# Performance work log

Measured on AMD Instinct MI355X. Metric: run time of the kernel, lower is better.

The kernel has to match this reference:

```python
import jax, jax.numpy as jnp
import numpy as np

K = 10      # neighbors; conv width math 10 -> 3 -> 1
EPS = 1e-5  # InstanceNorm2d default eps (affine=False)
NEG = 0.2   # leaky relu slope


def _instnorm(x):
    m = x.mean(axis=(2, 3), keepdims=True)
    v = x.var(axis=(2, 3), keepdims=True)  # biased var, as in torch instance_norm
    return (x - m) * jax.lax.rsqrt(v + EPS)


def _conv13(x, w, b, s):
    y = jax.lax.conv_general_dilated(x, w, (1, s), 'VALID',
                                     dimension_numbers=('NCHW', 'OIHW', 'NCHW'))
    return y + b[None, :, None, None]


def _block(x, wA, bA, wB, bB):
    # Sequential(conv(1,3,stride(1,3)), IN, ReLU, conv(1,3), IN, ReLU)
    y = jax.nn.relu(_instnorm(_conv13(x, wA, bA, 3)))
    return jax.nn.relu(_instnorm(_conv13(y, wB, bB, 1)))


def _knn_idx(coords, k):
    # coords [B,2,N] -> k nearest neighbor indices [B,N,k] (self excluded)
    pts = coords.transpose(0, 2, 1)
    sq = (pts ** 2).sum(-1)
    dist = sq[:, :, None] + sq[:, None, :] - 2.0 * jnp.einsum('bnc,bmc->bnm', pts, pts)
    dist = jnp.clip(dist, 1e-12)
    _, idx = jax.lax.top_k(-dist, k + 1)  # smallest distances, sorted
    return idx[:, :, 1:]


def _gather_nb(x, idx):
    # x [B,C,N], idx [B,N,k] -> [B,C,N,k]
    return jax.vmap(lambda f, i: f[:, i])(x, idx)


def _graph_feat(feats, idx):
    nb = _gather_nb(feats, idx)
    ctr = jnp.broadcast_to(feats[..., None], nb.shape)
    return jnp.concatenate([ctr, nb - ctr], axis=1)  # [B,2C,N,k]


def _cos_angle(coords, idx):
    nei = _gather_nb(coords, idx)          # [B,2,N,k]
    ctr = coords[..., None]                # [B,2,N,1]
    dot = (ctr * nei).sum(axis=1, keepdims=True)
    na = jnp.sqrt((ctr ** 2).sum(axis=1, keepdims=True))
    nb = jnp.sqrt((nei ** 2).sum(axis=1, keepdims=True))
    return dot / (na * nb)                 # [B,1,N,k]


def _c1(w, x):
    # 1x1 conv, no bias
    return jnp.einsum('oi,bihw->bohw', w, x)


def _forward(coords, features, W1, W2, W3, W3o, a1wA, a1bA, a1wB, a1bB,
             a2wA, a2bA, a2wB, a2bB, angwA, angbA, angwB, angbB):
    B, C, N = features.shape
    lrelu = lambda x: jax.nn.leaky_relu(x, NEG)
    x0 = features[..., None]
    # KNN depends only on coords: all three torch graph builds give identical indices
    idx = _knn_idx(coords, K)
    x1_old = _graph_feat(features, idx)                         # [B,2C,N,K]
    x1 = _block(x1_old, a1wA, a1bA, a1wB, a1bB)                 # [B,C,N,1]
    # angle_enc1 is shared and idx identical -> f_ang1 == f_ang2
    f_ang = _block(_cos_angle(coords, idx), angwA, angbA, angwB, angbB)
    x2 = _block(_graph_feat(x1[..., 0], idx), a2wA, a2bA, a2wB, a2bB)
    x3 = jnp.concatenate([x0, x1 + f_ang, x2 + f_ang], axis=1)  # [B,3C,N,1]
    x3 = lrelu(_instnorm(_c1(W3, x3))).reshape(B, -1, N)
    x1o = lrelu(_instnorm(_c1(W1, x1_old))).max(axis=-1, keepdims=True)   # [B,C,N,1]
    x2o = lrelu(_instnorm(_c1(W2, _graph_feat(x1o[..., 0], idx)))).max(axis=-1, keepdims=True)
    x3o = jnp.concatenate([x0, x1o, x2o], axis=1)               # [B,4C,N,1]
    x3o = lrelu(_instnorm(_c1(W3o, x3o))).reshape(B, -1, N)
    return x3 + x3o


def setup_inputs():
    key = jax.random.key(0)
    ks = jax.random.split(key, 20)
    B, C, N = 4, 128, 4096
    r = lambda i, shp, sc=1.0: jax.random.normal(ks[i], shp, jnp.float32) * sc
    s = 0.05
    return {
        'coords': r(0, (B, 2, N)),
        'features': r(1, (B, C, N)),
        'W1': r(2, (C, 2 * C), s),
        'W2': r(3, (2 * C, 2 * C), s),
        'W3': r(4, (C, 3 * C), s),
        'W3o': r(5, (C, 4 * C), s),
        'a1wA': r(6, (C, 2 * C, 1, 3), s), 'a1bA': r(7, (C,), s),
        'a1wB': r(8, (C, C, 1, 3), s), 'a1bB': r(9, (C,), s),
        'a2wA': r(10, (C, 2 * C, 1, 3), s), 'a2bA': r(11, (C,), s),
        'a2wB': r(12, (C, C, 1, 3), s), 'a2bB': r(13, (C,), s),
        'angwA': r(14, (C, 1, 1, 3), s), 'angbA': r(15, (C,), s),
        'angwB': r(16, (C, C, 1, 3), s), 'angbB': r(17, (C,), s),
    }


def reference(coords, features, W1, W2, W3, W3o, a1wA, a1bA, a1wB, a1bB,
              a2wA, a2bA, a2wB, a2bB, angwA, angbA, angwB, angbB):
    return _forward(coords, features, W1, W2, W3, W3o, a1wA, a1bA, a1wB, a1bB,
                    a2wA, a2bA, a2wB, a2bB, angwA, angbA, angwB, angbB)
```

## Files before the change

kernel.cpp:

```cpp
#include <hip/hip_runtime.h>
#include <hip/hip_bf16.h>

typedef unsigned long long ull;

#define BN 4
#define CH 128
#define NP 4096
#define KNB 10
#define EPSI 1e-5f
#define GM_PTS 16
#define CA_PTS 8

#define FMA4(A, W, F) do { (A).x += (W).x*(F); (A).y += (W).y*(F); \
                           (A).z += (W).z*(F); (A).w += (W).w*(F); } while(0)

__device__ __forceinline__ ull shfl_xor_u64(ull v, int mask) {
    unsigned lo = (unsigned)(v & 0xFFFFFFFFu);
    unsigned hi = (unsigned)(v >> 32);
    lo = __shfl_xor(lo, mask);
    hi = __shfl_xor(hi, mask);
    return ((ull)hi << 32) | lo;
}

__device__ __forceinline__ int clampj(int j) { return ((unsigned)j < (unsigned)NP) ? j : 0; }

__device__ __forceinline__ void d_packA(const float* w, float* WT, int i) {
    int co = i % CH, ci = (i / CH) % CH, s = i / (CH * CH);
    float val;
    if (s == 0) {
        val = 0.f;
        for (int dk = 0; dk < 3; dk++)
            val += w[(co * 256 + ci) * 3 + dk] - w[(co * 256 + 128 + ci) * 3 + dk];
    } else {
        val = w[(co * 256 + 128 + ci) * 3 + (s - 1)];
    }
    WT[i] = val;
}
__device__ __forceinline__ void d_packB(const float* w, float* WT, int i) {
    int co = i % CH, ci = (i / CH) % CH, dk = i / (CH * CH);
    WT[i] = w[(co * CH + ci) * 3 + dk];
}
__device__ __forceinline__ void d_packUV(const float* w, float* Wu, float* Wn, int Cout, int i) {
    int co = i % Cout, ci = i / Cout;
    float a = w[co * 256 + ci], bb = w[co * 256 + 128 + ci];
    Wu[i] = a - bb; Wn[i] = bb;
}
__device__ __forceinline__ void d_packP(const float* w, float* WT, int Cin, int Cout, int i) {
    int co = i % Cout, ci = i / Cout;
    WT[i] = w[co * Cin + ci];
}

__global__ void pack_all(const float* __restrict__ a1wA, const float* __restrict__ a2wA,
                         const float* __restrict__ a1wB, const float* __restrict__ a2wB,
                         const float* __restrict__ angwB, const float* __restrict__ W1,
                         const float* __restrict__ W2, const float* __restrict__ W3,
                         const float* __restrict__ W3o, const float* __restrict__ angwA,
                         float* __restrict__ WA1T, float* __restrict__ WA2T,
                         float* __restrict__ WB1T, float* __restrict__ WB2T,
                         float* __restrict__ WBAT,
                         float* __restrict__ W1U, float* __restrict__ W1N,
                         float* __restrict__ W2U, float* __restrict__ W2N,
                         float* __restrict__ W3T, float* __restrict__ W3OT,
                         float* __restrict__ WANGA) {
    int i = blockIdx.x * 256 + threadIdx.x;
    const int sA = 4 * CH * CH;
    const int sB = 3 * CH * CH;
    if (i < sA) { d_packA(a1wA, WA1T, i); return; } i -= sA;
    if (i < sA) { d_packA(a2wA, WA2T, i); return; } i -= sA;
    if (i < sB) { d_packB(a1wB, WB1T, i); return; } i -= sB;
    if (i < sB) { d_packB(a2wB, WB2T, i); return; } i -= sB;
    if (i < sB) { d_packB(angwB, WBAT, i); return; } i -= sB;
    if (i < CH * CH) { d_packUV(W1, W1U, W1N, CH, i); return; } i -= CH * CH;
    if (i < CH * 256) { d_packUV(W2, W2U, W2N, 256, i); return; } i -= CH * 256;
    if (i < 384 * CH) { d_packP(W3, W3T, 384, CH, i); return; } i -= 384 * CH;
    if (i < 512 * CH) { d_packP(W3o, W3OT, 512, CH, i); return; } i -= 512 * CH;
    if (i < 3 * CH) { d_packP(angwA, WANGA, 3, CH, i); return; }
}

__global__ void ftrans_kernel(const float* __restrict__ feats, float* __restrict__ F) {
    int i = blockIdx.x * 256 + threadIdx.x;
    if (i >= BN * CH * NP) return;
    int n = i % NP, c = (i / NP) % CH, b = i / (NP * CH);
    F[(b * NP + n) * CH + c] = feats[i];
}

__global__ void knn_kernel(const float* __restrict__ coords, int* __restrict__ IDX) {
    int gw = blockIdx.x * 4 + (threadIdx.x >> 6);
    int b = gw / NP;
    int n = gw % NP;
    int lane = threadIdx.x & 63;
    float xn = coords[(b * 2 + 0) * NP + n];
    float yn = coords[(b * 2 + 1) * NP + n];
    float sn = __fadd_rn(__fmul_rn(xn, xn), __fmul_rn(yn, yn));
    ull a[11];
    #pragma unroll
    for (int q = 0; q < 11; q++) a[q] = 0xFFFFFFFFFFFFFFFFULL;
    for (int m = lane; m < NP; m += 64) {
        float xm = coords[(b * 2 + 0) * NP + m];
        float ym = coords[(b * 2 + 1) * NP + m];
        float sm = __fadd_rn(__fmul_rn(xm, xm), __fmul_rn(ym, ym));
        float dot = __fmaf_rn(yn, ym, __fmul_rn(xn, xm));
        float d = __fsub_rn(__fadd_rn(sn, sm), __fmul_rn(2.0f, dot));
        d = fmaxf(d, 1e-12f);
        ull key = ((ull)__float_as_uint(d) << 32) | (unsigned)m;
        if (key < a[10]) {
            a[10] = key;
            #pragma unroll
            for (int q = 10; q > 0; --q)
                if (a[q] < a[q - 1]) { ull t = a[q]; a[q] = a[q - 1]; a[q - 1] = t; }
        }
    }
    for (int r = 0; r < 11; ++r) {
        ull k = a[0];
        ull mk = k;
        #pragma unroll
        for (int off = 1; off < 64; off <<= 1) {
            ull o = shfl_xor_u64(mk, off);
            mk = (o < mk) ? o : mk;
        }
        if (k == mk) {
            #pragma unroll
            for (int q = 0; q < 10; ++q) a[q] = a[q + 1];
            a[10] = 0xFFFFFFFFFFFFFFFFULL;
        }
        if (lane == 0 && r > 0) IDX[(b * NP + n) * KNB + (r - 1)] = (int)(mk & 0xFFFFFFFFu);
    }
}

__global__ void cosangle_kernel(const float* __restrict__ coords, const int* __restrict__ IDX,
                                float* __restrict__ COSA) {
    int i = blockIdx.x * 256 + threadIdx.x;
    if (i >= BN * NP * KNB) return;
    int n = (i / KNB) % NP, b = i / (KNB * NP);
    int j = clampj(IDX[i]);
    float xc = coords[(b * 2 + 0) * NP + n], yc = coords[(b * 2 + 1) * NP + n];
    float xm = coords[(b * 2 + 0) * NP + j], ym = coords[(b * 2 + 1) * NP + j];
    float dot = xc * xm + yc * ym;
    float na = sqrtf(xc * xc + yc * yc);
    float nb2 = sqrtf(xm * xm + ym * ym);
    COSA[i] = dot / fmaxf(na * nb2, 1e-30f);
}

__global__ __launch_bounds__(256) void convA_kernel(const float* __restrict__ Fin,
                             const int* __restrict__ IDX,
                             const float* __restrict__ WT, float* __restrict__ YA,
                             float* __restrict__ PART,
                             const float* __restrict__ STATS, int slot) {
    __shared__ __align__(16) float ctr[CA_PTS][CH];
    __shared__ __align__(16) float nb[CA_PTS][9][CH];
    __shared__ int jidx[CA_PTS * 9];
    int b = blockIdx.x / (NP / CA_PTS);
    int chunk = blockIdx.x % (NP / CA_PTS);
    int n0 = chunk * CA_PTS;
    int cog = threadIdx.x & 31;
    int pg  = threadIdx.x >> 5;
    const float* SB = (slot >= 0) ? &STATS[((size_t)(slot * BN + b) * 256) * 2] : nullptr;
    if (threadIdx.x < CA_PTS * 9) {
        int n = threadIdx.x / 9, kk = threadIdx.x % 9;
        jidx[threadIdx.x] = clampj(IDX[(b * NP + n0 + n) * KNB + kk]);
    }
    __syncthreads();
    {
        int v4 = threadIdx.x;
        int n = v4 >> 5, c4 = v4 & 31;
        float4 x = *(const float4*)&Fin[(size_t)(b * NP + n0 + n) * CH + c4 * 4];
        if (SB) {
            float4 s0 = *(const float4*)&SB[c4 * 8];
            float4 s1 = *(const float4*)&SB[c4 * 8 + 4];
            x.x = fmaxf((x.x - s0.x) * s0.y, 0.f);
            x.y = fmaxf((x.y - s0.z) * s0.w, 0.f);
            x.z = fmaxf((x.z - s1.x) * s1.y, 0.f);
            x.w = fmaxf((x.w - s1.z) * s1.w, 0.f);
        }
        *(float4*)&ctr[n][c4 * 4] = x;
    }
    for (int v4 = threadIdx.x; v4 < CA_PTS * 9 * 32; v4 += 256) {
        int n = v4 / 288, rem = v4 % 288, kk = rem >> 5, c4 = rem & 31;
        float4 x = *(const float4*)&Fin[(size_t)(b * NP + jidx[n * 9 + kk]) * CH + c4 * 4];
        if (SB) {
            float4 s0 = *(const float4*)&SB[c4 * 8];
            float4 s1 = *(const float4*)&SB[c4 * 8 + 4];
            x.x = fmaxf((x.x - s0.x) * s0.y, 0.f);
            x.y = fmaxf((x.y - s0.z) * s0.w, 0.f);
            x.z = fmaxf((x.z - s1.x) * s1.y, 0.f);
            x.w = fmaxf((x.w - s1.z) * s1.w, 0.f);
        }
        *(float4*)&nb[n][kk][c4 * 4] = x;
    }
    __syncthreads();
    const float4* W4 = (const float4*)WT;
    float4 cacc; cacc.x = cacc.y = cacc.z = cacc.w = 0.f;
    {
        const float* xb = &ctr[pg][0];
        for (int ci = 0; ci < CH; ci += 4) {
            float4 x = *(const float4*)&xb[ci];
            #pragma unroll
            for (int u = 0; u < 4; ++u) {
                float4 w = W4[(ci + u) * 32 + cog];
                float f = ((const float*)&x)[u];
                FMA4(cacc, w, f);
            }
        }
    }
    float4 t0 = cacc, t1 = cacc, t2 = cacc;
    for (int dk = 0; dk < 3; ++dk) {
        const float4* Wd = W4 + (size_t)(1 + dk) * (CH * 32);
        const float* b0 = &nb[pg][0 * 3 + dk][0];
        const float* b1 = &nb[pg][1 * 3 + dk][0];
        const float* b2 = &nb[pg][2 * 3 + dk][0];
        for (int ci = 0; ci < CH; ci += 4) {
            float4 x0 = *(const float4*)&b0[ci];
            float4 x1 = *(const float4*)&b1[ci];
            float4 x2 = *(const float4*)&b2[ci];
            #pragma unroll
            for (int u = 0; u < 4; ++u) {
                float4 w = Wd[(ci + u) * 32 + cog];
                float f0 = ((const float*)&x0)[u];
                float f1 = ((const float*)&x1)[u];
                float f2 = ((const float*)&x2)[u];
                FMA4(t0, w, f0); FMA4(t1, w, f1); FMA4(t2, w, f2);
            }
        }
    }
    {
        size_t base = ((size_t)(b * NP + n0 + pg) * 3) * CH + cog * 4;
        *(float4*)&YA[base + 0 * CH] = t0;
        *(float4*)&YA[base + 1 * CH] = t1;
        *(float4*)&YA[base + 2 * CH] = t2;
    }
    float s4[4], q4[4];
    s4[0] = t0.x + t1.x + t2.x; q4[0] = t0.x*t0.x + t1.x*t1.x + t2.x*t2.x;
    s4[1] = t0.y + t1.y + t2.y; q4[1] = t0.y*t0.y + t1.y*t1.y + t2.y*t2.y;
    s4[2] = t0.z + t1.z + t2.z; q4[2] = t0.z*t0.z + t1.z*t1.z + t2.z*t2.z;
    s4[3] = t0.w + t1.w + t2.w; q4[3] = t0.w*t0.w + t1.w*t1.w + t2.w*t2.w;
    __syncthreads();
    float* red = &nb[0][0][0];
    #pragma unroll
    for (int j = 0; j < 4; ++j) {
        red[((pg * 32 + cog) * 4 + j) * 2 + 0] = s4[j];
        red[((pg * 32 + cog) * 4 + j) * 2 + 1] = q4[j];
    }
    __syncthreads();
    if (threadIdx.x < CH) {
        int c = threadIdx.x;
        float ss = 0.f, qq = 0.f;
        #pragma unroll
        for (int g = 0; g < 8; ++g) {
            ss += red[((g * 32 + (c >> 2)) * 4 + (c & 3)) * 2 + 0];
            qq += red[((g * 32 + (c >> 2)) * 4 + (c & 3)) * 2 + 1];
        }
        PART[((size_t)(b * (NP / CA_PTS) + chunk) * 256 + c) * 2 + 0] = ss;
        PART[((size_t)(b * (NP / CA_PTS) + chunk) * 256 + c) * 2 + 1] = qq;
    }
}

__global__ void angA_kernel(const float* __restrict__ COSA, const float* __restrict__ WT,
                            float* __restrict__ YA, float* __restrict__ PART) {
    __shared__ float ca[32][10];
    int b = blockIdx.x / (NP / 32);
    int chunk = blockIdx.x % (NP / 32);
    int n0 = chunk * 32;
    int co = threadIdx.x;
    for (int v = threadIdx.x; v < 320; v += 128) {
        int nn = v / 10, kk = v % 10;
        ca[nn][kk] = COSA[(b * NP + n0 + nn) * KNB + kk];
    }
    float w0 = WT[co], w1 = WT[CH + co], w2 = WT[2 * CH + co];
    __syncthreads();
    float sum = 0.f, sq = 0.f;
    for (int nn = 0; nn < 32; nn++) {
        #pragma unroll
        for (int t = 0; t < 3; t++) {
            float v = w0 * ca[nn][3 * t] + w1 * ca[nn][3 * t + 1] + w2 * ca[nn][3 * t + 2];
            YA[((b * NP + n0 + nn) * 3 + t) * CH + co] = v;
            sum += v; sq += v * v;
        }
    }
    PART[((b * (NP / 32) + chunk) * 256 + co) * 2 + 0] = sum;
    PART[((b * (NP / 32) + chunk) * 256 + co) * 2 + 1] = sq;
}

template <int CIN, int NCOG>
__device__ __forceinline__ void gemm_16pt(const float* lds, const float* __restrict__ WT,
                                          int cog, int pg, float4 acc[4]) {
    const float4* W4 = (const float4*)WT;
    const float* xb = lds + pg * 4 * CIN;
    for (int ci = 0; ci < CIN; ci += 4) {
        float4 x0 = *(const float4*)&xb[0 * CIN + ci];
        float4 x1 = *(const float4*)&xb[1 * CIN + ci];
        float4 x2 = *(const float4*)&xb[2 * CIN + ci];
        float4 x3 = *(const float4*)&xb[3 * CIN + ci];
        #pragma unroll
        for (int u = 0; u < 4; ++u) {
            float4 w = W4[(ci + u) * NCOG + cog];
            float f0 = ((const float*)&x0)[u];
            float f1 = ((const float*)&x1)[u];
            float f2 = ((const float*)&x2)[u];
            float f3 = ((const float*)&x3)[u];
            FMA4(acc[0], w, f0); FMA4(acc[1], w, f1);
            FMA4(acc[2], w, f2); FMA4(acc[3], w, f3);
        }
    }
}

template <int NCOG>
__device__ __forceinline__ void reduce_stats(const float* s4, const float* q4,
                                             float* red, float* __restrict__ PART,
                                             int b, int chunk, int nchunks,
                                             int pg, int cog) {
    constexpr int COUT = NCOG * 4;
    __syncthreads();
    #pragma unroll
    for (int j = 0; j < 4; ++j) {
        red[((pg * NCOG + cog) * 4 + j) * 2 + 0] = s4[j];
        red[((pg * NCOG + cog) * 4 + j) * 2 + 1] = q4[j];
    }
    __syncthreads();
    int c = threadIdx.x;
    if (c < COUT) {
        float ss = 0.f, qq = 0.f;
        #pragma unroll
        for (int g = 0; g < 4; ++g) {
            ss += red[((g * NCOG + (c >> 2)) * 4 + (c & 3)) * 2 + 0];
            qq += red[((g * NCOG + (c >> 2)) * 4 + (c & 3)) * 2 + 1];
        }
        PART[((size_t)(b * nchunks + chunk) * 256 + c) * 2 + 0] = ss;
        PART[((size_t)(b * nchunks + chunk) * 256 + c) * 2 + 1] = qq;
    }
}

template <int NCOG>
__device__ __forceinline__ void out16(const float4 acc[4], float* __restrict__ OUT,
                                      int b, int n0, int pg, int cog,
                                      float s4[4], float q4[4]) {
    constexpr int COUT = NCOG * 4;
    #pragma unroll
    for (int p = 0; p < 4; ++p) {
        *(float4*)&OUT[(size_t)(b * NP + n0 + pg * 4 + p) * COUT + cog * 4] = acc[p];
        s4[0] += acc[p].x; s4[1] += acc[p].y; s4[2] += acc[p].z; s4[3] += acc[p].w;
        q4[0] += acc[p].x * acc[p].x; q4[1] += acc[p].y * acc[p].y;
        q4[2] += acc[p].z * acc[p].z; q4[3] += acc[p].w * acc[p].w;
    }
}

template <int CIN, int NCOG>
__global__ void pixel_gemm_t(const float* __restrict__ IN_, const float* __restrict__ WT,
                             float* __restrict__ OUT, const float* __restrict__ STATS,
                             int slot, int act, float* __restrict__ PART) {
    constexpr int COUT = NCOG * 4;
    constexpr int BD = 4 * NCOG;
    __shared__ __align__(16) float ldsin[16 * CIN];
    int b = blockIdx.x / (NP / 16);
    int chunk = blockIdx.x % (NP / 16);
    int n0 = chunk * 16;
    int cog = threadIdx.x & (NCOG - 1);
    int pg = threadIdx.x / NCOG;
    constexpr int nv4 = 16 * CIN / 4;
    if (slot >= 0) {
        int cbase = (4 * threadIdx.x) & 127;
        const float* st = &STATS[((slot * BN + b) * 256 + cbase) * 2];
        float m0 = st[0], r0 = st[1], m1 = st[2], r1 = st[3];
        float m2 = st[4], r2 = st[5], m3 = st[6], r3 = st[7];
        for (int v4 = threadIdx.x; v4 < nv4; v4 += BD) {
            float4 x = *(const float4*)&IN_[(size_t)(b * NP + n0) * CIN + 4 * v4];
            float v0 = (x.x - m0) * r0, v1 = (x.y - m1) * r1;
            float v2 = (x.z - m2) * r2, v3 = (x.w - m3) * r3;
            if (act) {
                x.x = (v0 >= 0.f) ? v0 : 0.2f * v0;
                x.y = (v1 >= 0.f) ? v1 : 0.2f * v1;
                x.z = (v2 >= 0.f) ? v2 : 0.2f * v2;
                x.w = (v3 >= 0.f) ? v3 : 0.2f * v3;
            } else {
                x.x = fmaxf(v0, 0.f); x.y = fmaxf(v1, 0.f);
                x.z = fmaxf(v2, 0.f); x.w = fmaxf(v3, 0.f);
            }
            *(float4*)&ldsin[4 * v4] = x;
        }
    } else {
        for (int v4 = threadIdx.x; v4 < nv4; v4 += BD)
            *(float4*)&ldsin[4 * v4] =
                *(const float4*)&IN_[(size_t)(b * NP + n0) * CIN + 4 * v4];
    }
    __syncthreads();
    float4 acc[4];
    #pragma unroll
    for (int p = 0; p < 4; ++p) acc[p].x = acc[p].y = acc[p].z = acc[p].w = 0.f;
    gemm_16pt<CIN, NCOG>(ldsin, WT, cog, pg, acc);
    float s4[4] = {0,0,0,0}, q4[4] = {0,0,0,0};
    out16<NCOG>(acc, OUT, b, n0, pg, cog, s4, q4);
    if (PART)
        reduce_stats<NCOG>(s4, q4, ldsin, PART, b, chunk, NP / 16, pg, cog);
}

__global__ void stats_final(const float* __restrict__ PART, float* __restrict__ STATS,
                            int S, int Cc, int slot, int nch) {
    __shared__ float ssum[256], ssq[256];
    int bc = blockIdx.x;
    int b = bc / Cc, c = bc % Cc;
    float sum = 0.f, sq = 0.f;
    for (int ch = threadIdx.x; ch < nch; ch += 256) {
        sum += PART[((b * nch + ch) * 256 + c) * 2 + 0];
        sq  += PART[((b * nch + ch) * 256 + c) * 2 + 1];
    }
    ssum[threadIdx.x] = sum; ssq[threadIdx.x] = sq;
    __syncthreads();
    for (int s = 128; s > 0; s >>= 1) {
        if (threadIdx.x < s) {
            ssum[threadIdx.x] += ssum[threadIdx.x + s];
            ssq[threadIdx.x]  += ssq[threadIdx.x + s];
        }
        __syncthreads();
    }
    if (threadIdx.x == 0) {
        float mean = ssum[0] / (float)S;
        float var = fmaxf(ssq[0] / (float)S - mean * mean, 0.f);
        STATS[((slot * BN + b) * 256 + c) * 2 + 0] = mean;
        STATS[((slot * BN + b) * 256 + c) * 2 + 1] = rsqrtf(var + EPSI);
    }
}

template <int NCOG>
__global__ void gathermax_t(const float* __restrict__ X, const float* __restrict__ Wu,
                            const float* __restrict__ V, const int* __restrict__ IDX,
                            float* __restrict__ M, float* __restrict__ PART,
                            const float* __restrict__ STATS, int slot) {
    constexpr int COUT = NCOG * 4;
    __shared__ __align__(16) float rows[GM_PTS * CH];
    int b = blockIdx.x / (NP / GM_PTS);
    int chunk = blockIdx.x % (NP / GM_PTS);
    int n0 = chunk * GM_PTS;
    int cog = threadIdx.x & (NCOG - 1);
    int pg = threadIdx.x / NCOG;
    if (slot >= 0) {
        int c0 = (4 * threadIdx.x) & 127;
        const float* st = &STATS[((slot * BN + b) * 256 + c0) * 2];
        float m0 = st[0], r0 = st[1], m1 = st[2], r1 = st[3];
        float m2 = st[4], r2 = st[5], m3 = st[6], r3 = st[7];
        for (int v4 = threadIdx.x; v4 < GM_PTS * CH / 4; v4 += COUT) {
            float4 x = *(const float4*)&X[(size_t)(b * NP + n0) * CH + v4 * 4];
            float v0 = (x.x - m0) * r0, v1 = (x.y - m1) * r1;
            float v2 = (x.z - m2) * r2, v3 = (x.w - m3) * r3;
            x.x = (v0 >= 0.f) ? v0 : 0.2f * v0;
            x.y = (v1 >= 0.f) ? v1 : 0.2f * v1;
            x.z = (v2 >= 0.f) ? v2 : 0.2f * v2;
            x.w = (v3 >= 0.f) ? v3 : 0.2f * v3;
            *(float4*)&rows[v4 * 4] = x;
        }
    } else {
        for (int v4 = threadIdx.x; v4 < GM_PTS * CH / 4; v4 += COUT)
            *(float4*)&rows[v4 * 4] = *(const float4*)&X[(size_t)(b * NP + n0) * CH + v4 * 4];
    }
    __syncthreads();
    float4 acc[4];
    #pragma unroll
    for (int p = 0; p < 4; ++p) acc[p].x = acc[p].y = acc[p].z = acc[p].w = 0.f;
    gemm_16pt<CH, NCOG>(rows, Wu, cog, pg, acc);
    float s4[4] = {0,0,0,0}, q4[4] = {0,0,0,0};
    #pragma unroll
    for (int p = 0; p < 4; ++p) {
        int nn = n0 + pg * 4 + p;
        float4 u = acc[p];
        float4 best; best.x = best.y = best.z = best.w = -3.4e38f;
        for (int k = 0; k < KNB; ++k) {
            int j = clampj(IDX[(b * NP + nn) * KNB + k]);
            float4 vv = *(const float4*)&V[(size_t)(b * NP + j) * COUT + cog * 4];
            vv.x += u.x; vv.y += u.y; vv.z += u.z; vv.w += u.w;
            s4[0] += vv.x; s4[1] += vv.y; s4[2] += vv.z; s4[3] += vv.w;
            q4[0] += vv.x * vv.x; q4[1] += vv.y * vv.y;
            q4[2] += vv.z * vv.z; q4[3] += vv.w * vv.w;
            best.x = fmaxf(best.x, vv.x); best.y = fmaxf(best.y, vv.y);
            best.z = fmaxf(best.z, vv.z); best.w = fmaxf(best.w, vv.w);
        }
        *(float4*)&M[(size_t)(b * NP + nn) * COUT + cog * 4] = best;
    }
    __syncthreads();
    reduce_stats<NCOG>(s4, q4, rows, PART, b, chunk, NP / GM_PTS, pg, cog);
}

__global__ void head3_kernel(const float* __restrict__ F, const float* __restrict__ X1,
                             const float* __restrict__ X2, const float* __restrict__ FANG,
                             const float* __restrict__ WT, float* __restrict__ Y3,
                             float* __restrict__ PART, const float* __restrict__ STATS) {
    __shared__ __align__(16) float lds[16 * 384];
    int b = blockIdx.x / (NP / 16);
    int chunk = blockIdx.x % (NP / 16);
    int n0 = chunk * 16;
    int cog = threadIdx.x & 31;
    int pg = threadIdx.x >> 5;
    const float* S1 = &STATS[((size_t)(1 * BN + b) * 256) * 2];
    const float* S5 = &STATS[((size_t)(5 * BN + b) * 256) * 2];
    const float* S3 = &STATS[((size_t)(3 * BN + b) * 256) * 2];
    for (int v4 = threadIdx.x; v4 < 16 * 96; v4 += 128) {
        int nn = v4 / 96, q4 = v4 % 96;
        int part = q4 >> 5, c4 = q4 & 31;
        size_t base = (size_t)(b * NP + n0 + nn) * CH + c4 * 4;
        float4 val;
        if (part == 0) val = *(const float4*)&F[base];
        else {
            const float* src = (part == 1) ? X1 : X2;
            const float* SX = (part == 1) ? S1 : S5;
            float4 xx = *(const float4*)&src[base];
            float4 aa = *(const float4*)&FANG[base];
            float4 sx0 = *(const float4*)&SX[c4 * 8];
            float4 sx1 = *(const float4*)&SX[c4 * 8 + 4];
            float4 sa0 = *(const float4*)&S3[c4 * 8];
            float4 sa1 = *(const float4*)&S3[c4 * 8 + 4];
            val.x = fmaxf((xx.x - sx0.x) * sx0.y, 0.f) + fmaxf((aa.x - sa0.x) * sa0.y, 0.f);
            val.y = fmaxf((xx.y - sx0.z) * sx0.w, 0.f) + fmaxf((aa.y - sa0.z) * sa0.w, 0.f);
            val.z = fmaxf((xx.z - sx1.x) * sx1.y, 0.f) + fmaxf((aa.z - sa1.x) * sa1.y, 0.f);
            val.w = fmaxf((xx.w - sx1.z) * sx1.w, 0.f) + fmaxf((aa.w - sa1.z) * sa1.w, 0.f);
        }
        *(float4*)&lds[v4 * 4] = val;
    }
    __syncthreads();
    float4 acc[4];
    #pragma unroll
    for (int p = 0; p < 4; ++p) acc[p].x = acc[p].y = acc[p].z = acc[p].w = 0.f;
    gemm_16pt<384, 32>(lds, WT, cog, pg, acc);
    float s4[4] = {0,0,0,0}, q4[4] = {0,0,0,0};
    out16<32>(acc, Y3, b, n0, pg, cog, s4, q4);
    reduce_stats<32>(s4, q4, lds, PART, b, chunk, NP / 16, pg, cog);
}

__global__ void head3o_kernel(const float* __restrict__ F, const float* __restrict__ X1O,
                              const float* __restrict__ X2O, const float* __restrict__ WT,
                              float* __restrict__ Y3O, float* __restrict__ PART,
                              const float* __restrict__ STATS) {
    __shared__ __align__(16) float lds[16 * 512];
    int b = blockIdx.x / (NP / 16);
    int chunk = blockIdx.x % (NP / 16);
    int n0 = chunk * 16;
    int cog = threadIdx.x & 31;
    int pg = threadIdx.x >> 5;
    const float* S6 = &STATS[((size_t)(6 * BN + b) * 256) * 2];
    const float* S7 = &STATS[((size_t)(7 * BN + b) * 256) * 2];
    for (int v4 = threadIdx.x; v4 < 16 * 128; v4 += 128) {
        int nn = v4 >> 7, q4 = v4 & 127;
        float4 val;
        if (q4 < 32) {
            val = *(const float4*)&F[(size_t)(b * NP + n0 + nn) * CH + q4 * 4];
        } else if (q4 < 64) {
            int c4 = q4 - 32;
            float4 x = *(const float4*)&X1O[(size_t)(b * NP + n0 + nn) * CH + c4 * 4];
            float4 s0 = *(const float4*)&S6[c4 * 8];
            float4 s1 = *(const float4*)&S6[c4 * 8 + 4];
            float v0 = (x.x - s0.x) * s0.y, v1 = (x.y - s0.z) * s0.w;
            float v2 = (x.z - s1.x) * s1.y, v3 = (x.w - s1.z) * s1.w;
            val.x = (v0 >= 0.f) ? v0 : 0.2f * v0;
            val.y = (v1 >= 0.f) ? v1 : 0.2f * v1;
            val.z = (v2 >= 0.f) ? v2 : 0.2f * v2;
            val.w = (v3 >= 0.f) ? v3 : 0.2f * v3;
        } else {
            int c4 = q4 - 64;
            float4 x = *(const float4*)&X2O[(size_t)(b * NP + n0 + nn) * 256 + c4 * 4];
            float4 s0 = *(const float4*)&S7[c4 * 8];
            float4 s1 = *(const float4*)&S7[c4 * 8 + 4];
            float v0 = (x.x - s0.x) * s0.y, v1 = (x.y - s0.z) * s0.w;
            float v2 = (x.z - s1.x) * s1.y, v3 = (x.w - s1.z) * s1.w;
            val.x = (v0 >= 0.f) ? v0 : 0.2f * v0;
            val.y = (v1 >= 0.f) ? v1 : 0.2f * v1;
            val.z = (v2 >= 0.f) ? v2 : 0.2f * v2;
            val.w = (v3 >= 0.f) ? v3 : 0.2f * v3;
        }
        *(float4*)&lds[v4 * 4] = val;
    }
    __syncthreads();
    float4 acc[4];
    #pragma unroll
    for (int p = 0; p < 4; ++p) acc[p].x = acc[p].y = acc[p].z = acc[p].w = 0.f;
    gemm_16pt<512, 32>(lds, WT, cog, pg, acc);
    float s4[4] = {0,0,0,0}, q4[4] = {0,0,0,0};
    out16<32>(acc, Y3O, b, n0, pg, cog, s4, q4);
    reduce_stats<32>(s4, q4, lds, PART, b, chunk, NP / 16, pg, cog);
}

__global__ void final_kernel(const float* __restrict__ Y3, const float* __restrict__ Y3O,
                             const float* __restrict__ STATS, float* __restrict__ out) {
    __shared__ float T[64][129];
    int b = blockIdx.x / (NP / 64);
    int n0 = (blockIdx.x % (NP / 64)) * 64;
    int co = threadIdx.x;
    float m3 = STATS[((8 * BN + b) * 256 + co) * 2 + 0];
    float r3 = STATS[((8 * BN + b) * 256 + co) * 2 + 1];
    float m3o = STATS[((9 * BN + b) * 256 + co) * 2 + 0];
    float r3o = STATS[((9 * BN + b) * 256 + co) * 2 + 1];
    for (int j = 0; j < 64; j++) {
        size_t idx = (size_t)(b * NP + n0 + j) * CH + co;
        float v3 = (Y3[idx] - m3) * r3;
        v3 = (v3 >= 0.f) ? v3 : 0.2f * v3;
        float v3o = (Y3O[idx] - m3o) * r3o;
        v3o = (v3o >= 0.f) ? v3o : 0.2f * v3o;
        T[j][co] = v3 + v3o;
    }
    __syncthreads();
    for (int rr = 0; rr < 64; rr++) {
        int r = rr * 2 + (threadIdx.x >> 6);
        int j = threadIdx.x & 63;
        out[(size_t)(b * CH + r) * NP + n0 + j] = T[j][r];
    }
}

extern "C" void kernel_launch(void* const* d_in, const int* in_sizes, int n_in,
                              void* d_out, int out_size, void* d_ws, size_t ws_size,
                              hipStream_t stream) {
    const float* coords   = (const float*)d_in[0];
    const float* features = (const float*)d_in[1];
    const float* W1   = (const float*)d_in[2];
    const float* W2   = (const float*)d_in[3];
    const float* W3   = (const float*)d_in[4];
    const float* W3o  = (const float*)d_in[5];
    const float* a1wA = (const float*)d_in[6];
    const float* a1wB = (const float*)d_in[8];
    const float* a2wA = (const float*)d_in[10];
    const float* a2wB = (const float*)d_in[12];
    const float* angwA = (const float*)d_in[14];
    const float* angwB = (const float*)d_in[16];
    float* out = (float*)d_out;
    float* ws = (float*)d_ws;
    (void)ws_size; (void)in_sizes; (void)n_in; (void)out_size;

    size_t off = 0;
    float* WA1T  = ws + off; off += 4 * CH * CH;
    float* WA2T  = ws + off; off += 4 * CH * CH;
    float* WB1T  = ws + off; off += 3 * CH * CH;
    float* WB2T  = ws + off; off += 3 * CH * CH;
    float* WBAT  = ws + off; off += 3 * CH * CH;
    float* WANGA = ws + off; off += 512;
    float* W1U   = ws + off; off += CH * CH;
    float* W1N   = ws + off; off += CH * CH;
    float* W2U   = ws + off; off += CH * 256;
    float* W2N   = ws + off; off += CH * 256;
    float* W3T   = ws + off; off += 384 * CH;
    float* W3OT  = ws + off; off += 512 * CH;
    int*   IDX   = (int*)(ws + off); off += (size_t)BN * NP * KNB;
    float* COSA  = ws + off; off += (size_t)BN * NP * KNB;
    float* PART  = ws + off; off += (size_t)BN * 1024 * 256 * 2;
    float* STATS = ws + off; off += 10 * BN * 256 * 2;
    const size_t UNIT = (size_t)BN * NP * CH;
    float* POOL  = ws + off; off += 7 * UNIT;

    float* F    = POOL + 0 * UNIT;
    float* YA   = POOL + 1 * UNIT;
    float* X1   = POOL + 4 * UNIT;
    float* FANG = POOL + 5 * UNIT;
    float* X2   = POOL + 6 * UNIT;
    float* Y3   = POOL + 1 * UNIT;
    float* V1   = POOL + 2 * UNIT;
    float* M1   = POOL + 6 * UNIT;
    float* V2   = POOL + 4 * UNIT;
    float* M2   = POOL + 2 * UNIT;
    float* Y3O  = POOL + 4 * UNIT;

    pack_all<<<1730, 256, 0, stream>>>(a1wA, a2wA, a1wB, a2wB, angwB, W1, W2, W3, W3o, angwA,
                                       WA1T, WA2T, WB1T, WB2T, WBAT,
                                       W1U, W1N, W2U, W2N, W3T, W3OT, WANGA);

    ftrans_kernel<<<(BN * CH * NP + 255) / 256, 256, 0, stream>>>(features, F);
    knn_kernel<<<BN * NP / 4, 256, 0, stream>>>(coords, IDX);
    cosangle_kernel<<<(BN * NP * KNB + 255) / 256, 256, 0, stream>>>(coords, IDX, COSA);

    auto sfin = [&](int S, int Cc, int slot, int nch) {
        stats_final<<<BN * Cc, 256, 0, stream>>>(PART, STATS, S, Cc, slot, nch);
    };

    convA_kernel<<<BN * (NP / CA_PTS), 256, 0, stream>>>(F, IDX, WA1T, YA, PART, STATS, -1);
    sfin(3 * NP, CH, 0, NP / CA_PTS);
    pixel_gemm_t<384, 32><<<BN * (NP / 16), 128, 0, stream>>>(YA, WB1T, X1, STATS, 0, 0, PART);
    sfin(NP, CH, 1, NP / 16);

    angA_kernel<<<BN * (NP / 32), 128, 0, stream>>>(COSA, WANGA, YA, PART);
    sfin(3 * NP, CH, 2, NP / 32);
    pixel_gemm_t<384, 32><<<BN * (NP / 16), 128, 0, stream>>>(YA, WBAT, FANG, STATS, 2, 0, PART);
    sfin(NP, CH, 3, NP / 16);

    convA_kernel<<<BN * (NP / CA_PTS), 256, 0, stream>>>(X1, IDX, WA2T, YA, PART, STATS, 1);
    sfin(3 * NP, CH, 4, NP / CA_PTS);
    pixel_gemm_t<384, 32><<<BN * (NP / 16), 128, 0, stream>>>(YA, WB2T, X2, STATS, 4, 0, PART);
    sfin(NP, CH, 5, NP / 16);

    head3_kernel<<<BN * (NP / 16), 128, 0, stream>>>(F, X1, X2, FANG, W3T, Y3, PART, STATS);
    sfin(NP, CH, 8, NP / 16);

    pixel_gemm_t<128, 32><<<BN * (NP / 16), 128, 0, stream>>>(F, W1N, V1, STATS, -1, 0, nullptr);
    gathermax_t<32><<<BN * (NP / GM_PTS), 128, 0, stream>>>(F, W1U, V1, IDX, M1, PART, STATS, -1);
    sfin(NP * KNB, CH, 6, NP / GM_PTS);

    pixel_gemm_t<128, 64><<<BN * (NP / 16), 256, 0, stream>>>(M1, W2N, V2, STATS, 6, 1, nullptr);
    gathermax_t<64><<<BN * (NP / GM_PTS), 256, 0, stream>>>(M1, W2U, V2, IDX, M2, PART, STATS, 6);
    sfin(NP * KNB, 256, 7, NP / GM_PTS);

    head3o_kernel<<<BN * (NP / 16), 128, 0, stream>>>(F, M1, M2, W3OT, Y3O, PART, STATS);
    sfin(NP, CH, 9, NP / 16);
    final_kernel<<<BN * (NP / 64), 128, 0, stream>>>(Y3, Y3O, STATS, out);
}
```

Before: 905.5 us.

## Prune KNN scan with warp threshold; double points per convA block with bf16 neighbors

The KNN scan now computes a wavefront-wide minimum of each lane's 11th-best key every 8 iterations and skips insertions that cannot enter the global top-11, which cuts divergent sort work. convA now handles 16 points per block, with each thread computing two points so every weight load feeds twice as many FMAs. Neighbor features are stored in shared memory as bf16 to keep the larger tile's LDS footprint manageable. This adds bf16 rounding to the neighbor inputs of the conv, a precision change, and doubles per-thread register use. The partial-stats layout also depends on NP/CA_PTS, so the code not shown must follow the new chunk count.

```diff
diff --git a/kernel.cpp b/kernel.cpp
--- a/kernel.cpp
+++ b/kernel.cpp
@@ -9,7 +9,7 @@
 #define KNB 10
 #define EPSI 1e-5f
 #define GM_PTS 16
-#define CA_PTS 8
+#define CA_PTS 16
 
 #define FMA4(A, W, F) do { (A).x += (W).x*(F); (A).y += (W).y*(F); \
                            (A).z += (W).z*(F); (A).w += (W).w*(F); } while(0)
@@ -23,6 +23,20 @@
 }
 
 __device__ __forceinline__ int clampj(int j) { return ((unsigned)j < (unsigned)NP) ? j : 0; }
+
+__device__ __forceinline__ unsigned short f2bf(float f) {
+    unsigned u = __float_as_uint(f);
+    unsigned r = u + 0x7FFFu + ((u >> 16) & 1u);
+    return (unsigned short)(r >> 16);
+}
+__device__ __forceinline__ float bf2f(unsigned short h) {
+    return __uint_as_float(((unsigned)h) << 16);
+}
+__device__ __forceinline__ float4 bfload4(const unsigned short* p) {
+    ushort4 h = *(const ushort4*)p;
+    float4 r; r.x = bf2f(h.x); r.y = bf2f(h.y); r.z = bf2f(h.z); r.w = bf2f(h.w);
+    return r;
+}
 
 __device__ __forceinline__ void d_packA(const float* w, float* WT, int i) {
     int co = i % CH, ci = (i / CH) % CH, s = i / (CH * CH);
@@ -95,7 +109,9 @@
     ull a[11];
     #pragma unroll
     for (int q = 0; q < 11; q++) a[q] = 0xFFFFFFFFFFFFFFFFULL;
-    for (int m = lane; m < NP; m += 64) {
+    ull T = 0xFFFFFFFFFFFFFFFFULL;
+    for (int it = 0; it < NP / 64; ++it) {
+        int m = lane + (it << 6);
         float xm = coords[(b * 2 + 0) * NP + m];
         float ym = coords[(b * 2 + 1) * NP + m];
         float sm = __fadd_rn(__fmul_rn(xm, xm), __fmul_rn(ym, ym));
@@ -103,11 +119,20 @@
         float d = __fsub_rn(__fadd_rn(sn, sm), __fmul_rn(2.0f, dot));
         d = fmaxf(d, 1e-12f);
         ull key = ((ull)__float_as_uint(d) << 32) | (unsigned)m;
-        if (key < a[10]) {
+        if (key < a[10] && key < T) {
             a[10] = key;
             #pragma unroll
             for (int q = 10; q > 0; --q)
                 if (a[q] < a[q - 1]) { ull t = a[q]; a[q] = a[q - 1]; a[q - 1] = t; }
+        }
+        if ((it & 7) == 7) {
+            ull t = a[10];
+            #pragma unroll
+            for (int off = 1; off < 64; off <<= 1) {
+                ull o = shfl_xor_u64(t, off);
+                t = (o < t) ? o : t;
+            }
+            T = t;
         }
     }
     for (int r = 0; r < 11; ++r) {
@@ -147,7 +172,7 @@
                              float* __restrict__ PART,
                              const float* __restrict__ STATS, int slot) {
     __shared__ __align__(16) float ctr[CA_PTS][CH];
-    __shared__ __align__(16) float nb[CA_PTS][9][CH];
+    __shared__ __align__(16) unsigned short nbh[CA_PTS][9][CH];
     __shared__ int jidx[CA_PTS * 9];
     int b = blockIdx.x / (NP / CA_PTS);
     int chunk = blockIdx.x % (NP / CA_PTS);
@@ -160,8 +185,7 @@
         jidx[threadIdx.x] = clampj(IDX[(b * NP + n0 + n) * KNB + kk]);
     }
     __syncthreads();
-    {
-        int v4 = threadIdx.x;
+    for (int v4 = threadIdx.x; v4 < CA_PTS * 32; v4 += 256) {
         int n = v4 >> 5, c4 = v4 & 31;
         float4 x = *(const float4*)&Fin[(size_t)(b * NP + n0 + n) * CH + c4 * 4];
         if (SB) {
@@ -185,56 +209,77 @@
             x.z = fmaxf((x.z - s1.x) * s1.y, 0.f);
             x.w = fmaxf((x.w - s1.z) * s1.w, 0.f);
         }
-        *(float4*)&nb[n][kk][c4 * 4] = x;
+        ushort4 h;
+        h.x = f2bf(x.x); h.y = f2bf(x.y); h.z = f2bf(x.z); h.w = f2bf(x.w);
+        *(ushort4*)&nbh[n][kk][c4 * 4] = h;
     }
     __syncthreads();
     const float4* W4 = (const float4*)WT;
-    float4 cacc; cacc.x = cacc.y = cacc.z = cacc.w = 0.f;
-    {
-        const float* xb = &ctr[pg][0];
-        for (int ci = 0; ci < CH; ci += 4) {
-            float4 x = *(const float4*)&xb[ci];
-            #pragma unroll
-            for (int u = 0; u < 4; ++u) {
-                float4 w = W4[(ci + u) * 32 + cog];
-                float f = ((const float*)&x)[u];
-                FMA4(cacc, w, f);
-            }
-        }
-    }
-    float4 t0 = cacc, t1 = cacc, t2 = cacc;
+    const int p0 = pg * 2, p1 = pg * 2 + 1;
+    float4 cacc0, cacc1;
+    cacc0.x = cacc0.y = cacc0.z = cacc0.w = 0.f;
+    cacc1 = cacc0;
+    for (int ci = 0; ci < CH; ci += 4) {
+        float4 xa = *(const float4*)&ctr[p0][ci];
+        float4 xb = *(const float4*)&ctr[p1][ci];
+        #pragma unroll
+        for (int u = 0; u < 4; ++u) {
+            float4 w = W4[(ci + u) * 32 + cog];
+            float fa = ((const float*)&xa)[u];
+            float fb = ((const float*)&xb)[u];
+            FMA4(cacc0, w, fa); FMA4(cacc1, w, fb);
+        }
+    }
+    float4 t00 = cacc0, t01 = cacc0, t02 = cacc0;
+    float4 t10 = cacc1, t11 = cacc1, t12 = cacc1;
     for (int dk = 0; dk < 3; ++dk) {
         const float4* Wd = W4 + (size_t)(1 + dk) * (CH * 32);
-        const float* b0 = &nb[pg][0 * 3 + dk][0];
-        const float* b1 = &nb[pg][1 * 3 + dk][0];
-        const float* b2 = &nb[pg][2 * 3 + dk][0];
+        const unsigned short* a00 = &nbh[p0][0 * 3 + dk][0];
+        const unsigned short* a01 = &nbh[p0][1 * 3 + dk][0];
+        const unsigned short* a02 = &nbh[p0][2 * 3 + dk][0];
+        const unsigned short* a10 = &nbh[p1][0 * 3 + dk][0];
+        const unsigned short* a11 = &nbh[p1][1 * 3 + dk][0];
+        const unsigned short* a12 = &nbh[p1][2 * 3 + dk][0];
         for (int ci = 0; ci < CH; ci += 4) {
-            float4 x0 = *(const float4*)&b0[ci];
-            float4 x1 = *(const float4*)&b1[ci];
-            float4 x2 = *(const float4*)&b2[ci];
+            float4 x00 = bfload4(&a00[ci]);
+            float4 x01 = bfload4(&a01[ci]);
+            float4 x02 = bfload4(&a02[ci]);
+            float4 x10 = bfload4(&a10[ci]);
+            float4 x11 = bfload4(&a11[ci]);
+            float4 x12 = bfload4(&a12[ci]);
             #pragma unroll
             for (int u = 0; u < 4; ++u) {
                 float4 w = Wd[(ci + u) * 32 + cog];
-                float f0 = ((const float*)&x0)[u];
-                float f1 = ((const float*)&x1)[u];
-                float f2 = ((const float*)&x2)[u];
-                FMA4(t0, w, f0); FMA4(t1, w, f1); FMA4(t2, w, f2);
+                FMA4(t00, w, ((const float*)&x00)[u]);
+                FMA4(t01, w, ((const float*)&x01)[u]);
+                FMA4(t02, w, ((const float*)&x02)[u]);
+                FMA4(t10, w, ((const float*)&x10)[u]);
+                FMA4(t11, w, ((const float*)&x11)[u]);
+                FMA4(t12, w, ((const float*)&x12)[u]);
             }
         }
     }
     {
-        size_t base = ((size_t)(b * NP + n0 + pg) * 3) * CH + cog * 4;
-        *(float4*)&YA[base + 0 * CH] = t0;
-        *(float4*)&YA[base + 1 * CH] = t1;
-        *(float4*)&YA[base + 2 * CH] = t2;
+        size_t base0 = ((size_t)(b * NP + n0 + p0) * 3) * CH + cog * 4;
+        *(float4*)&YA[base0 + 0 * CH] = t00;
+        *(float4*)&YA[base0 + 1 * CH] = t01;
+        *(float4*)&YA[base0 + 2 * CH] = t02;
+        size_t base1 = ((size_t)(b * NP + n0 + p1) * 3) * CH + cog * 4;
+        *(float4*)&YA[base1 + 0 * CH] = t10;
+        *(float4*)&YA[base1 + 1 * CH] = t11;
+        *(float4*)&YA[base1 + 2 * CH] = t12;
     }
     float s4[4], q4[4];
-    s4[0] = t0.x + t1.x + t2.x; q4[0] = t0.x*t0.x + t1.x*t1.x + t2.x*t2.x;
-    s4[1] = t0.y + t1.y + t2.y; q4[1] = t0.y*t0.y + t1.y*t1.y + t2.y*t2.y;
-    s4[2] = t0.z + t1.z + t2.z; q4[2] = t0.z*t0.z + t1.z*t1.z + t2.z*t2.z;
-    s4[3] = t0.w + t1.w + t2.w; q4[3] = t0.w*t0.w + t1.w*t1.w + t2.w*t2.w;
-    __syncthreads();
-    float* red = &nb[0][0][0];
+    s4[0] = t00.x + t01.x + t02.x + t10.x + t11.x + t12.x;
+    s4[1] = t00.y + t01.y + t02.y + t10.y + t11.y + t12.y;
+    s4[2] = t00.z + t01.z + t02.z + t10.z + t11.z + t12.z;
+    s4[3] = t00.w + t01.w + t02.w + t10.w + t11.w + t12.w;
+    q4[0] = t00.x*t00.x + t01.x*t01.x + t02.x*t02.x + t10.x*t10.x + t11.x*t11.x + t12.x*t12.x;
+    q4[1] = t00.y*t00.y + t01.y*t01.y + t02.y*t02.y + t10.y*t10.y + t11.y*t11.y + t12.y*t12.y;
+    q4[2] = t00.z*t00.z + t01.z*t01.z + t02.z*t02.z + t10.z*t10.z + t11.z*t11.z + t12.z*t12.z;
+    q4[3] = t00.w*t00.w + t01.w*t01.w + t02.w*t02.w + t10.w*t10.w + t11.w*t11.w + t12.w*t12.w;
+    __syncthreads();
+    float* red = (float*)&nbh[0][0][0];
     #pragma unroll
     for (int j = 0; j < 4; ++j) {
         red[((pg * 32 + cog) * 4 + j) * 2 + 0] = s4[j];
```

Result: faster. 851.4 us (-6.0%).
